# Performance work log

Hardware: AMD Instinct MI355X
Metric: run time of the kernel (lower is better)

Reference implementation:

```python
import jax, jax.numpy as jnp
import numpy as np

B, T, N = 32, 24, 512
DIM_IN, DIM_OUT, HID, EMB = 64, 2, 128, 16
NEG_SLOPE = 0.01  # nn.LeakyReLU default


def leaky_relu(x):
    return jnp.where(x >= 0, x, NEG_SLOPE * x)


def setup_inputs() -> dict:
    key = jax.random.key(0)
    ks = jax.random.split(key, 11)
    return {
        "eb": jax.random.normal(ks[0], (B, T, N, DIM_IN), jnp.float32),
        "time_eb": jax.random.normal(ks[1], (B, T, EMB), jnp.float32),
        "node_eb": jax.random.normal(ks[2], (N, EMB), jnp.float32),
        # ln1: Linear(dim_in, hidden) stored as [dim_in, hidden] (x @ W + b)
        "W1": jax.random.normal(ks[3], (DIM_IN, HID), jnp.float32) / np.sqrt(DIM_IN),
        "b1": jax.random.normal(ks[4], (HID,), jnp.float32) * 0.01,
        # ln3: Linear(hidden, dim_out)
        "W3": jax.random.normal(ks[5], (HID, DIM_OUT), jnp.float32) / np.sqrt(HID),
        "b3": jax.random.normal(ks[6], (DIM_OUT,), jnp.float32) * 0.01,
        "weights_pool_spa": jax.random.normal(ks[7], (EMB, HID, HID), jnp.float32),
        "bias_pool_spa": jax.random.normal(ks[8], (EMB, HID), jnp.float32),
        "weights_pool_tem": jax.random.normal(ks[9], (EMB, HID, HID), jnp.float32),
        "bias_pool_tem": jax.random.normal(ks[10], (EMB, HID), jnp.float32),
    }


def reference(eb, time_eb, node_eb, W1, b1, W3, b3,
              weights_pool_spa, bias_pool_spa,
              weights_pool_tem, bias_pool_tem):
    # eb: [b,t,n,dim_in] -> [b,t,n,hidden]
    eb_out = eb @ W1 + b1
    # spatial hypernetwork: per-node weight [n,hid,hid] and bias [n,hid]
    weights_spa = jnp.einsum('nd,dio->nio', node_eb, weights_pool_spa)
    bias_spa = node_eb @ bias_pool_spa  # [n,hid]
    out_spa = leaky_relu(jnp.einsum('btni,nio->btno', eb_out, weights_spa) + bias_spa)
    # temporal hypernetwork: per-(b,t) weight [b,t,hid,hid] and bias [b,t,1,hid]
    weights_tem = jnp.einsum('btd,dio->btio', time_eb, weights_pool_tem)
    bias_tem = (time_eb @ bias_pool_tem)[:, :, None, :]
    out_tem = leaky_relu(jnp.einsum('btni,btio->btno', out_spa, weights_tem) + bias_tem)
    logits = out_tem @ W3 + b3  # [b,t,n,dim_out]
    return logits
```

## Files before the change

### kernel.cpp

```cpp
#include <hip/hip_runtime.h>
#include <hip/hip_bf16.h>
#include <stdint.h>

#define BT   768
#define NN   512
#define DIN  64
#define HID  128
#define EMB  16
#define SLOPE 0.01f

typedef __attribute__((ext_vector_type(8))) short bf16x8;
typedef __attribute__((ext_vector_type(4))) float f32x4;
typedef __attribute__((ext_vector_type(4))) short short4v;

__device__ __forceinline__ short f2bf(float f) {
    uint32_t u = __float_as_uint(f);
    u += 0x7fff + ((u >> 16) & 1);
    return (short)(u >> 16);
}
__device__ __forceinline__ float bf2f(short s) {
    return __uint_as_float(((uint32_t)(unsigned short)s) << 16);
}

static const size_t OFF_PTT  = 0;
static const size_t OFF_PTS2 = 524288;
static const size_t OFF_QB   = 786432;
static const size_t OFF_H2   = 1048576;

__global__ __launch_bounds__(256)
void k_prep(const float* __restrict__ pool_spa, const float* __restrict__ pool_tem,
            const float* __restrict__ W1, const float* __restrict__ b1,
            const float* __restrict__ bp_spa,
            short* __restrict__ ptt, short* __restrict__ pts2,
            float* __restrict__ qb)
{
    const int b = blockIdx.x, t = threadIdx.x;
    __shared__ short smem[26112];

    if (b < 64) {
        const int d = b >> 2, o0 = (b & 3) * 32;
        short* s = smem;
        #pragma unroll
        for (int c = 0; c < 16; ++c) {
            int e = c * 256 + t;
            int i = e >> 5, oo = e & 31;
            s[oo * 136 + i] = f2bf(pool_tem[(d * HID + i) * HID + o0 + oo]);
        }
        __syncthreads();
        #pragma unroll
        for (int c = 0; c < 8; ++c) {
            int e = c * 256 + t;
            int oo = e >> 6, ii = (e & 63) * 2;
            uint32_t lo = (unsigned short)s[oo * 136 + ii];
            uint32_t hi = (unsigned short)s[oo * 136 + ii + 1];
            ((uint32_t*)ptt)[((d * HID + o0 + oo) * HID + ii) >> 1] = lo | (hi << 16);
        }
        return;
    }
    if (b < 66) {
        const int dbase = (b - 64) * 8;
        if (t < 128) {
            float a[8];
            #pragma unroll
            for (int dd = 0; dd < 8; ++dd) a[dd] = bp_spa[(dbase + dd) * HID + t];
            for (int i = 0; i < HID; ++i) {
                float bv = b1[i];
                #pragma unroll
                for (int dd = 0; dd < 8; ++dd)
                    a[dd] += bv * pool_spa[((dbase + dd) * HID + i) * HID + t];
            }
            #pragma unroll
            for (int dd = 0; dd < 8; ++dd) qb[(dbase + dd) * HID + t] = a[dd];
        }
        return;
    }
    {
        const int d = b - 66;
        const int wave = t >> 6, lane = t & 63, quad = lane >> 4, l15 = lane & 15;
        const int m0 = wave * 32;
        short* sPT  = smem;
        short* sW1b = smem + 128 * 136;
        #pragma unroll
        for (int c = 0; c < 64; ++c) {
            int idx = c * 256 + t;
            int i = idx >> 7, o = idx & 127;
            sPT[o * 136 + i] = f2bf(pool_spa[(d * HID + i) * HID + o]);
        }
        #pragma unroll
        for (int c = 0; c < 32; ++c) {
            int idx = c * 256 + t;
            sW1b[(idx >> 7) * 136 + (idx & 127)] = f2bf(W1[idx]);
        }
        __syncthreads();
        f32x4 acc[2][4] = {};
        #pragma unroll
        for (int kc = 0; kc < 4; ++kc) {
            bf16x8 a0 = *(const bf16x8*)(sPT + (m0 + l15) * 136 + kc * 32 + quad * 8);
            bf16x8 a1 = *(const bf16x8*)(sPT + (m0 + 16 + l15) * 136 + kc * 32 + quad * 8);
            #pragma unroll
            for (int tc = 0; tc < 4; ++tc) {
                bf16x8 bb = *(const bf16x8*)(sW1b + (tc * 16 + l15) * 136 + kc * 32 + quad * 8);
                acc[0][tc] = __builtin_amdgcn_mfma_f32_16x16x32_bf16(a0, bb, acc[0][tc], 0, 0, 0);
                acc[1][tc] = __builtin_amdgcn_mfma_f32_16x16x32_bf16(a1, bb, acc[1][tc], 0, 0, 0);
            }
        }
        __syncthreads();
        short* sO = smem;
        #pragma unroll
        for (int tr = 0; tr < 2; ++tr)
            #pragma unroll
            for (int tc = 0; tc < 4; ++tc)
                #pragma unroll
                for (int r = 0; r < 4; ++r)
                    sO[(m0 + tr * 16 + quad * 4 + r) * 72 + tc * 16 + l15] = f2bf(acc[tr][tc][r]);
        __syncthreads();
        #pragma unroll
        for (int c = 0; c < 4; ++c) {
            int idx = c * 256 + t;
            int row = idx >> 3, ko = (idx & 7) * 8;
            *(bf16x8*)(pts2 + (size_t)d * 8192 + row * 64 + ko) =
                *(const bf16x8*)(sO + row * 72 + ko);
        }
    }
}

__global__ __launch_bounds__(256)
void k_spatial(const float* __restrict__ eb, const short* __restrict__ pts2,
               const float* __restrict__ qb, const float* __restrict__ node_eb,
               short* __restrict__ h2)
{
    const int n = blockIdx.x;
    const int t = threadIdx.x;
    const int wave = t >> 6, lane = t & 63, quad = lane >> 4, l15 = lane & 15;
    const int m0 = (wave >> 1) * 32, n0 = (wave & 1) * 64;

    __shared__ short sW[128 * 72];
    __shared__ short sEb[2][64 * 72];
    __shared__ short sOut[2][64 * 136];

    const float* ebn = eb + (size_t)n * DIN;
    short* h2n = h2 + (size_t)n * (BT * HID);

    float4 ev[4];
    #pragma unroll
    for (int c = 0; c < 4; ++c) {
        int idx = c * 256 + t;
        int r = idx >> 4, kq = (idx & 15) * 4;
        ev[c] = *(const float4*)(ebn + (size_t)r * (NN * DIN) + kq);
    }
    float ne[EMB];
    #pragma unroll
    for (int d = 0; d < EMB; ++d) ne[d] = node_eb[n * EMB + d];
    float bsr[4];
    #pragma unroll
    for (int tc = 0; tc < 4; ++tc) {
        int col = n0 + tc * 16 + l15;
        float a = 0.f;
        #pragma unroll
        for (int d = 0; d < EMB; ++d) a += ne[d] * qb[d * HID + col];
        bsr[tc] = a;
    }
    #pragma unroll
    for (int c = 0; c < 4; ++c) {
        int idx = c * 256 + t;
        int o = idx >> 3, k0 = (idx & 7) * 8;
        float a8[8] = {};
        #pragma unroll
        for (int d = 0; d < EMB; ++d) {
            bf16x8 pv = *(const bf16x8*)(pts2 + (size_t)d * 8192 + o * 64 + k0);
            #pragma unroll
            for (int e = 0; e < 8; ++e) a8[e] += ne[d] * bf2f(pv[e]);
        }
        bf16x8 w;
        #pragma unroll
        for (int e = 0; e < 8; ++e) w[e] = f2bf(a8[e]);
        *(bf16x8*)(sW + o * 72 + k0) = w;
    }
    #pragma unroll
    for (int c = 0; c < 4; ++c) {
        int idx = c * 256 + t;
        int r = idx >> 4, kq = (idx & 15) * 4;
        short4v s;
        s.x = f2bf(ev[c].x); s.y = f2bf(ev[c].y);
        s.z = f2bf(ev[c].z); s.w = f2bf(ev[c].w);
        *(short4v*)(sEb[0] + r * 72 + kq) = s;
    }
    __syncthreads();

    for (int ch = 0; ch < 12; ++ch) {
        const int cur = ch & 1, nxt = cur ^ 1;
        if (ch < 11) {
            #pragma unroll
            for (int c = 0; c < 4; ++c) {
                int idx = c * 256 + t;
                int r = (ch + 1) * 64 + (idx >> 4), kq = (idx & 15) * 4;
                ev[c] = *(const float4*)(ebn + (size_t)r * (NN * DIN) + kq);
            }
        }
        f32x4 acc[2][4] = {};
        #pragma unroll
        for (int kc = 0; kc < 2; ++kc) {
            bf16x8 a0 = *(const bf16x8*)(sEb[cur] + (m0 + l15) * 72 + kc * 32 + quad * 8);
            bf16x8 a1 = *(const bf16x8*)(sEb[cur] + (m0 + 16 + l15) * 72 + kc * 32 + quad * 8);
            #pragma unroll
            for (int tc = 0; tc < 4; ++tc) {
                bf16x8 bfr = *(const bf16x8*)(sW + (n0 + tc * 16 + l15) * 72 + kc * 32 + quad * 8);
                acc[0][tc] = __builtin_amdgcn_mfma_f32_16x16x32_bf16(a0, bfr, acc[0][tc], 0, 0, 0);
                acc[1][tc] = __builtin_amdgcn_mfma_f32_16x16x32_bf16(a1, bfr, acc[1][tc], 0, 0, 0);
            }
        }
        #pragma unroll
        for (int tr = 0; tr < 2; ++tr)
            #pragma unroll
            for (int tc = 0; tc < 4; ++tc) {
                int col = n0 + tc * 16 + l15;
                #pragma unroll
                for (int r = 0; r < 4; ++r) {
                    float v = acc[tr][tc][r] + bsr[tc];
                    v = (v >= 0.f) ? v : SLOPE * v;
                    sOut[cur][(m0 + tr * 16 + quad * 4 + r) * 136 + col] = f2bf(v);
                }
            }
        if (ch < 11) {
            #pragma unroll
            for (int c = 0; c < 4; ++c) {
                int idx = c * 256 + t;
                int r = idx >> 4, kq = (idx & 15) * 4;
                short4v s;
                s.x = f2bf(ev[c].x); s.y = f2bf(ev[c].y);
                s.z = f2bf(ev[c].z); s.w = f2bf(ev[c].w);
                *(short4v*)(sEb[nxt] + r * 72 + kq) = s;
            }
        }
        __syncthreads();
        #pragma unroll
        for (int c = 0; c < 4; ++c) {
            int idx = c * 256 + t;
            *(bf16x8*)(h2n + (size_t)ch * (64 * HID) + (size_t)idx * 8) =
                *(const bf16x8*)(sOut[cur] + (idx >> 4) * 136 + (idx & 15) * 8);
        }
    }
}

__global__ __launch_bounds__(256, 3)
void k_temporal(const short* __restrict__ h2, const short* __restrict__ ptt,
                const float* __restrict__ bp_tem, const float* __restrict__ time_eb,
                const float* __restrict__ W3, const float* __restrict__ b3,
                float* __restrict__ out)
{
    const int R = blockIdx.x;
    const int t = threadIdx.x;
    const int wave = t >> 6, lane = t & 63, quad = lane >> 4, l15 = lane & 15;
    const int m0 = wave * 16;

    __shared__ short sWt[128 * 136];
    __shared__ short sH2[64 * 136];

    const short* hb = h2 + (size_t)R * HID;

    bf16x8 hreg[4];
    #pragma unroll
    for (int c = 0; c < 4; ++c) {
        int idx = c * 256 + t;
        hreg[c] = *(const bf16x8*)(hb + (size_t)(idx >> 4) * (BT * HID) + (idx & 15) * 8);
    }
    float te[EMB];
    #pragma unroll
    for (int d = 0; d < EMB; ++d) te[d] = time_eb[R * EMB + d];
    #pragma unroll
    for (int c = 0; c < 8; ++c) {
        int idx = c * 256 + t;
        int o = idx >> 4, i0 = (idx & 15) * 8;
        float a8[8] = {};
        #pragma unroll
        for (int d = 0; d < EMB; ++d) {
            bf16x8 pv = *(const bf16x8*)(ptt + (size_t)d * 16384 + o * 128 + i0);
            #pragma unroll
            for (int e = 0; e < 8; ++e) a8[e] += te[d] * bf2f(pv[e]);
        }
        bf16x8 w;
        #pragma unroll
        for (int e = 0; e < 8; ++e) w[e] = f2bf(a8[e]);
        *(bf16x8*)(sWt + o * 136 + i0) = w;
    }
    float btr[8], w3r0[8], w3r1[8];
    #pragma unroll
    for (int tc = 0; tc < 8; ++tc) {
        int o = tc * 16 + l15;
        float a = 0.f;
        #pragma unroll
        for (int d = 0; d < EMB; ++d) a += te[d] * bp_tem[d * HID + o];
        btr[tc] = a;
        w3r0[tc] = W3[2 * o]; w3r1[tc] = W3[2 * o + 1];
    }
    const float b30 = b3[0], b31 = b3[1];

    #pragma unroll
    for (int c = 0; c < 4; ++c) {
        int idx = c * 256 + t;
        *(bf16x8*)(sH2 + (idx >> 4) * 136 + (idx & 15) * 8) = hreg[c];
    }
    __syncthreads();

    for (int nt = 0; nt < 8; ++nt) {
        if (nt < 7) {
            #pragma unroll
            for (int c = 0; c < 4; ++c) {
                int idx = c * 256 + t;
                hreg[c] = *(const bf16x8*)(hb + (size_t)((nt + 1) * 64 + (idx >> 4)) * (BT * HID) + (idx & 15) * 8);
            }
        }
        f32x4 acc[8] = {};
        #pragma unroll
        for (int kc = 0; kc < 4; ++kc) {
            bf16x8 a = *(const bf16x8*)(sH2 + (m0 + l15) * 136 + kc * 32 + quad * 8);
            #pragma unroll
            for (int tc = 0; tc < 8; ++tc) {
                bf16x8 b = *(const bf16x8*)(sWt + (tc * 16 + l15) * 136 + kc * 32 + quad * 8);
                acc[tc] = __builtin_amdgcn_mfma_f32_16x16x32_bf16(a, b, acc[tc], 0, 0, 0);
            }
        }
        float pl[4][2] = {};
        #pragma unroll
        for (int tc = 0; tc < 8; ++tc) {
            #pragma unroll
            for (int r = 0; r < 4; ++r) {
                float v = acc[tc][r] + btr[tc];
                v = (v >= 0.f) ? v : SLOPE * v;
                pl[r][0] += v * w3r0[tc];
                pl[r][1] += v * w3r1[tc];
            }
        }
        #pragma unroll
        for (int m = 1; m <= 8; m <<= 1)
            #pragma unroll
            for (int r = 0; r < 4; ++r) {
                pl[r][0] += __shfl_xor(pl[r][0], m);
                pl[r][1] += __shfl_xor(pl[r][1], m);
            }
        if (l15 == 0) {
            #pragma unroll
            for (int r = 0; r < 4; ++r) {
                int nrow = nt * 64 + m0 + quad * 4 + r;
                *(float2*)(out + ((size_t)R * NN + nrow) * 2) =
                    make_float2(pl[r][0] + b30, pl[r][1] + b31);
            }
        }
        __syncthreads();
        if (nt < 7) {
            #pragma unroll
            for (int c = 0; c < 4; ++c) {
                int idx = c * 256 + t;
                *(bf16x8*)(sH2 + (idx >> 4) * 136 + (idx & 15) * 8) = hreg[c];
            }
            __syncthreads();
        }
    }
}

extern "C" void kernel_launch(void* const* d_in, const int* in_sizes, int n_in,
                              void* d_out, int out_size, void* d_ws, size_t ws_size,
                              hipStream_t stream) {
    const float* eb        = (const float*)d_in[0];
    const float* time_eb   = (const float*)d_in[1];
    const float* node_eb   = (const float*)d_in[2];
    const float* W1        = (const float*)d_in[3];
    const float* b1        = (const float*)d_in[4];
    const float* W3        = (const float*)d_in[5];
    const float* b3        = (const float*)d_in[6];
    const float* pool_spa  = (const float*)d_in[7];
    const float* bpool_spa = (const float*)d_in[8];
    const float* pool_tem  = (const float*)d_in[9];
    const float* bpool_tem = (const float*)d_in[10];
    float* out = (float*)d_out;

    char* ws = (char*)d_ws;
    short* ptt  = (short*)(ws + OFF_PTT);
    short* pts2 = (short*)(ws + OFF_PTS2);
    float* qb   = (float*)(ws + OFF_QB);
    short* h2   = (short*)(ws + OFF_H2);

    k_prep<<<82, 256, 0, stream>>>(pool_spa, pool_tem, W1, b1, bpool_spa,
                                   ptt, pts2, qb);
    k_spatial<<<dim3(NN), 256, 0, stream>>>(eb, pts2, qb, node_eb, h2);
    k_temporal<<<dim3(BT), 256, 0, stream>>>(h2, ptt, bpool_tem, time_eb, W3, b3, out);
}
```

Baseline: 243.1 us.

## Process two nodes per spatial block and split BT rows across two blocks

Each spatial block now covers two adjacent nodes and half of the 768 BT rows, so every eb row load fetches 128 contiguous floats (two nodes) instead of 64. Each wave pair owns one node's generated weight matrix, and the grid becomes 256x2. The cost is that per-node weight generation is repeated in both row-halves, and a second barrier per chunk is added.

```diff
diff --git a/kernel.cpp b/kernel.cpp
--- a/kernel.cpp
+++ b/kernel.cpp
@@ -129,61 +129,65 @@
                const float* __restrict__ qb, const float* __restrict__ node_eb,
                short* __restrict__ h2)
 {
-    const int n = blockIdx.x;
+    const int n0 = blockIdx.x * 2;
+    const int Rbase = blockIdx.y * 384;
     const int t = threadIdx.x;
     const int wave = t >> 6, lane = t & 63, quad = lane >> 4, l15 = lane & 15;
-    const int m0 = (wave >> 1) * 32, n0 = (wave & 1) * 64;
-
-    __shared__ short sW[128 * 72];
-    __shared__ short sEb[2][64 * 72];
-    __shared__ short sOut[2][64 * 136];
-
-    const float* ebn = eb + (size_t)n * DIN;
-    short* h2n = h2 + (size_t)n * (BT * HID);
+    const int wn = wave >> 1;
+    const int mrow = (wave & 1) * 16;
+
+    __shared__ short sW[2][128 * 72];
+    __shared__ short sEb[2][2][32 * 72];
+    __shared__ short sOut[2][32 * 136];
+
+    const float* ebn = eb + (size_t)n0 * DIN;
 
     float4 ev[4];
     #pragma unroll
     for (int c = 0; c < 4; ++c) {
         int idx = c * 256 + t;
-        int r = idx >> 4, kq = (idx & 15) * 4;
-        ev[c] = *(const float4*)(ebn + (size_t)r * (NN * DIN) + kq);
+        int r = idx >> 5, f4 = idx & 31;
+        ev[c] = *(const float4*)(ebn + (size_t)(Rbase + r) * (NN * DIN) + f4 * 4);
     }
     float ne[EMB];
     #pragma unroll
-    for (int d = 0; d < EMB; ++d) ne[d] = node_eb[n * EMB + d];
-    float bsr[4];
-    #pragma unroll
-    for (int tc = 0; tc < 4; ++tc) {
-        int col = n0 + tc * 16 + l15;
+    for (int d = 0; d < EMB; ++d) ne[d] = node_eb[(n0 + wn) * EMB + d];
+    float bsr[8];
+    #pragma unroll
+    for (int tc = 0; tc < 8; ++tc) {
+        int col = tc * 16 + l15;
         float a = 0.f;
         #pragma unroll
         for (int d = 0; d < EMB; ++d) a += ne[d] * qb[d * HID + col];
         bsr[tc] = a;
     }
+    {
+        const int pt = t & 127;
+        #pragma unroll
+        for (int c = 0; c < 8; ++c) {
+            int cell = c * 128 + pt;
+            int o = cell >> 3, k0 = (cell & 7) * 8;
+            float a8[8] = {};
+            #pragma unroll
+            for (int d = 0; d < EMB; ++d) {
+                bf16x8 pv = *(const bf16x8*)(pts2 + (size_t)d * 8192 + o * 64 + k0);
+                #pragma unroll
+                for (int e = 0; e < 8; ++e) a8[e] += ne[d] * bf2f(pv[e]);
+            }
+            bf16x8 w;
+            #pragma unroll
+            for (int e = 0; e < 8; ++e) w[e] = f2bf(a8[e]);
+            *(bf16x8*)(&sW[wn][o * 72 + k0]) = w;
+        }
+    }
     #pragma unroll
     for (int c = 0; c < 4; ++c) {
         int idx = c * 256 + t;
-        int o = idx >> 3, k0 = (idx & 7) * 8;
-        float a8[8] = {};
-        #pragma unroll
-        for (int d = 0; d < EMB; ++d) {
-            bf16x8 pv = *(const bf16x8*)(pts2 + (size_t)d * 8192 + o * 64 + k0);
-            #pragma unroll
-            for (int e = 0; e < 8; ++e) a8[e] += ne[d] * bf2f(pv[e]);
-        }
-        bf16x8 w;
-        #pragma unroll
-        for (int e = 0; e < 8; ++e) w[e] = f2bf(a8[e]);
-        *(bf16x8*)(sW + o * 72 + k0) = w;
-    }
-    #pragma unroll
-    for (int c = 0; c < 4; ++c) {
-        int idx = c * 256 + t;
-        int r = idx >> 4, kq = (idx & 15) * 4;
+        int r = idx >> 5, nn = (idx & 31) >> 4, k4 = (idx & 15) * 4;
         short4v s;
         s.x = f2bf(ev[c].x); s.y = f2bf(ev[c].y);
         s.z = f2bf(ev[c].z); s.w = f2bf(ev[c].w);
-        *(short4v*)(sEb[0] + r * 72 + kq) = s;
+        *(short4v*)(&sEb[0][nn][r * 72 + k4]) = s;
     }
     __syncthreads();
 
@@ -193,52 +197,51 @@
             #pragma unroll
             for (int c = 0; c < 4; ++c) {
                 int idx = c * 256 + t;
-                int r = (ch + 1) * 64 + (idx >> 4), kq = (idx & 15) * 4;
-                ev[c] = *(const float4*)(ebn + (size_t)r * (NN * DIN) + kq);
-            }
-        }
-        f32x4 acc[2][4] = {};
+                int r = (ch + 1) * 32 + (idx >> 5), f4 = idx & 31;
+                ev[c] = *(const float4*)(ebn + (size_t)(Rbase + r) * (NN * DIN) + f4 * 4);
+            }
+        }
+        f32x4 acc[8] = {};
         #pragma unroll
         for (int kc = 0; kc < 2; ++kc) {
-            bf16x8 a0 = *(const bf16x8*)(sEb[cur] + (m0 + l15) * 72 + kc * 32 + quad * 8);
-            bf16x8 a1 = *(const bf16x8*)(sEb[cur] + (m0 + 16 + l15) * 72 + kc * 32 + quad * 8);
-            #pragma unroll
-            for (int tc = 0; tc < 4; ++tc) {
-                bf16x8 bfr = *(const bf16x8*)(sW + (n0 + tc * 16 + l15) * 72 + kc * 32 + quad * 8);
-                acc[0][tc] = __builtin_amdgcn_mfma_f32_16x16x32_bf16(a0, bfr, acc[0][tc], 0, 0, 0);
-                acc[1][tc] = __builtin_amdgcn_mfma_f32_16x16x32_bf16(a1, bfr, acc[1][tc], 0, 0, 0);
-            }
-        }
-        #pragma unroll
-        for (int tr = 0; tr < 2; ++tr)
-            #pragma unroll
-            for (int tc = 0; tc < 4; ++tc) {
-                int col = n0 + tc * 16 + l15;
-                #pragma unroll
-                for (int r = 0; r < 4; ++r) {
-                    float v = acc[tr][tc][r] + bsr[tc];
-                    v = (v >= 0.f) ? v : SLOPE * v;
-                    sOut[cur][(m0 + tr * 16 + quad * 4 + r) * 136 + col] = f2bf(v);
-                }
-            }
+            bf16x8 a = *(const bf16x8*)(&sEb[cur][wn][(mrow + l15) * 72 + kc * 32 + quad * 8]);
+            #pragma unroll
+            for (int tc = 0; tc < 8; ++tc) {
+                bf16x8 bfr = *(const bf16x8*)(&sW[wn][(tc * 16 + l15) * 72 + kc * 32 + quad * 8]);
+                acc[tc] = __builtin_amdgcn_mfma_f32_16x16x32_bf16(a, bfr, acc[tc], 0, 0, 0);
+            }
+        }
+        #pragma unroll
+        for (int tc = 0; tc < 8; ++tc) {
+            int col = tc * 16 + l15;
+            #pragma unroll
+            for (int r = 0; r < 4; ++r) {
+                float v = acc[tc][r] + bsr[tc];
+                v = (v >= 0.f) ? v : SLOPE * v;
+                sOut[wn][(mrow + quad * 4 + r) * 136 + col] = f2bf(v);
+            }
+        }
         if (ch < 11) {
             #pragma unroll
             for (int c = 0; c < 4; ++c) {
                 int idx = c * 256 + t;
-                int r = idx >> 4, kq = (idx & 15) * 4;
+                int r = idx >> 5, nn = (idx & 31) >> 4, k4 = (idx & 15) * 4;
                 short4v s;
                 s.x = f2bf(ev[c].x); s.y = f2bf(ev[c].y);
                 s.z = f2bf(ev[c].z); s.w = f2bf(ev[c].w);
-                *(short4v*)(sEb[nxt] + r * 72 + kq) = s;
+                *(short4v*)(&sEb[nxt][nn][r * 72 + k4]) = s;
             }
         }
         __syncthreads();
         #pragma unroll
         for (int c = 0; c < 4; ++c) {
             int idx = c * 256 + t;
-            *(bf16x8*)(h2n + (size_t)ch * (64 * HID) + (size_t)idx * 8) =
-                *(const bf16x8*)(sOut[cur] + (idx >> 4) * 136 + (idx & 15) * 8);
-        }
+            int ni = idx >> 9, row = (idx & 511) >> 4, col8 = (idx & 15) * 8;
+            *(bf16x8*)(h2 + (size_t)(n0 + ni) * (BT * HID)
+                          + (size_t)(Rbase + ch * 32 + row) * HID + col8) =
+                *(const bf16x8*)(&sOut[ni][row * 136 + col8]);
+        }
+        __syncthreads();
     }
 }
 
@@ -382,6 +385,6 @@
 
     k_prep<<<82, 256, 0, stream>>>(pool_spa, pool_tem, W1, b1, bpool_spa,
                                    ptt, pts2, qb);
-    k_spatial<<<dim3(NN), 256, 0, stream>>>(eb, pts2, qb, node_eb, h2);
+    k_spatial<<<dim3(256, 2), 256, 0, stream>>>(eb, pts2, qb, node_eb, h2);
     k_temporal<<<dim3(BT), 256, 0, stream>>>(h2, ptt, bpool_tem, time_eb, W3, b3, out);
 }
```

New measurement: 247.8 us. No clear change (+2.0%).

## Split spatial and temporal stages by node halves and co-schedule them in one mixed kernel

Applied to the files above, without the earlier changes.

The spatial stage is split so each block handles half of the 768 (b,t) rows for one node, and the temporal stage is split into two node halves. The first node half of the spatial work, plus the pool_tem transpose, runs first. A mixed kernel then interleaves the remaining spatial blocks with temporal blocks for the already finished node half, and a final kernel runs temporal work for the second half. The aim is to fill the GPU better and overlap the two stages, at the price of generating each per-node and per-(b,t) hypernetwork weight twice and using larger shared-memory blocks.

```diff
diff --git a/kernel.cpp b/kernel.cpp
--- a/kernel.cpp
+++ b/kernel.cpp
@@ -27,38 +27,275 @@
 static const size_t OFF_QB   = 786432;
 static const size_t OFF_H2   = 1048576;
 
+
+__device__ __forceinline__ void spatial_block(
+    const float* __restrict__ eb, const short* __restrict__ pts2,
+    const float* __restrict__ qb, const float* __restrict__ node_eb,
+    short* __restrict__ h2, short* smem, int n, int Rbase)
+{
+    const int t = threadIdx.x;
+    const int wave = t >> 6, lane = t & 63, quad = lane >> 4, l15 = lane & 15;
+    const int m0 = (wave >> 1) * 32, n0 = (wave & 1) * 64;
+
+    short* sW    = smem;
+    short* sEbB  = smem + 9216;
+    short* sOutB = smem + 18432;
+
+    const float* ebn = eb + (size_t)n * DIN;
+    short* h2n = h2 + (size_t)n * (BT * HID) + (size_t)Rbase * HID;
+
+    float4 ev[4];
+    #pragma unroll
+    for (int c = 0; c < 4; ++c) {
+        int idx = c * 256 + t;
+        int r = idx >> 4, kq = (idx & 15) * 4;
+        ev[c] = *(const float4*)(ebn + (size_t)(Rbase + r) * (NN * DIN) + kq);
+    }
+    float ne[EMB];
+    #pragma unroll
+    for (int d = 0; d < EMB; ++d) ne[d] = node_eb[n * EMB + d];
+    float bsr[4];
+    #pragma unroll
+    for (int tc = 0; tc < 4; ++tc) {
+        int col = n0 + tc * 16 + l15;
+        float a = 0.f;
+        #pragma unroll
+        for (int d = 0; d < EMB; ++d) a += ne[d] * qb[d * HID + col];
+        bsr[tc] = a;
+    }
+    #pragma unroll
+    for (int c = 0; c < 4; ++c) {
+        int idx = c * 256 + t;
+        int o = idx >> 3, k0 = (idx & 7) * 8;
+        float a8[8] = {};
+        #pragma unroll
+        for (int d = 0; d < EMB; ++d) {
+            bf16x8 pv = *(const bf16x8*)(pts2 + (size_t)d * 8192 + o * 64 + k0);
+            #pragma unroll
+            for (int e = 0; e < 8; ++e) a8[e] += ne[d] * bf2f(pv[e]);
+        }
+        bf16x8 w;
+        #pragma unroll
+        for (int e = 0; e < 8; ++e) w[e] = f2bf(a8[e]);
+        *(bf16x8*)(sW + o * 72 + k0) = w;
+    }
+    #pragma unroll
+    for (int c = 0; c < 4; ++c) {
+        int idx = c * 256 + t;
+        int r = idx >> 4, kq = (idx & 15) * 4;
+        short4v s;
+        s.x = f2bf(ev[c].x); s.y = f2bf(ev[c].y);
+        s.z = f2bf(ev[c].z); s.w = f2bf(ev[c].w);
+        *(short4v*)(sEbB + r * 72 + kq) = s;
+    }
+    __syncthreads();
+
+    for (int ch = 0; ch < 6; ++ch) {
+        const int cur = ch & 1;
+        short* se  = sEbB + cur * 4608;
+        short* snx = sEbB + (cur ^ 1) * 4608;
+        short* so  = sOutB + cur * 8704;
+        if (ch < 5) {
+            #pragma unroll
+            for (int c = 0; c < 4; ++c) {
+                int idx = c * 256 + t;
+                int r = (ch + 1) * 64 + (idx >> 4), kq = (idx & 15) * 4;
+                ev[c] = *(const float4*)(ebn + (size_t)(Rbase + r) * (NN * DIN) + kq);
+            }
+        }
+        f32x4 acc[2][4] = {};
+        #pragma unroll
+        for (int kc = 0; kc < 2; ++kc) {
+            bf16x8 a0 = *(const bf16x8*)(se + (m0 + l15) * 72 + kc * 32 + quad * 8);
+            bf16x8 a1 = *(const bf16x8*)(se + (m0 + 16 + l15) * 72 + kc * 32 + quad * 8);
+            #pragma unroll
+            for (int tc = 0; tc < 4; ++tc) {
+                bf16x8 bfr = *(const bf16x8*)(sW + (n0 + tc * 16 + l15) * 72 + kc * 32 + quad * 8);
+                acc[0][tc] = __builtin_amdgcn_mfma_f32_16x16x32_bf16(a0, bfr, acc[0][tc], 0, 0, 0);
+                acc[1][tc] = __builtin_amdgcn_mfma_f32_16x16x32_bf16(a1, bfr, acc[1][tc], 0, 0, 0);
+            }
+        }
+        #pragma unroll
+        for (int tr = 0; tr < 2; ++tr)
+            #pragma unroll
+            for (int tc = 0; tc < 4; ++tc) {
+                int col = n0 + tc * 16 + l15;
+                #pragma unroll
+                for (int r = 0; r < 4; ++r) {
+                    float v = acc[tr][tc][r] + bsr[tc];
+                    v = (v >= 0.f) ? v : SLOPE * v;
+                    so[(m0 + tr * 16 + quad * 4 + r) * 136 + col] = f2bf(v);
+                }
+            }
+        if (ch < 5) {
+            #pragma unroll
+            for (int c = 0; c < 4; ++c) {
+                int idx = c * 256 + t;
+                int r = idx >> 4, kq = (idx & 15) * 4;
+                short4v s;
+                s.x = f2bf(ev[c].x); s.y = f2bf(ev[c].y);
+                s.z = f2bf(ev[c].z); s.w = f2bf(ev[c].w);
+                *(short4v*)(snx + r * 72 + kq) = s;
+            }
+        }
+        __syncthreads();
+        #pragma unroll
+        for (int c = 0; c < 4; ++c) {
+            int idx = c * 256 + t;
+            *(bf16x8*)(h2n + (size_t)ch * (64 * HID) + (size_t)idx * 8) =
+                *(const bf16x8*)(so + (idx >> 4) * 136 + (idx & 15) * 8);
+        }
+    }
+}
+
+__device__ __forceinline__ void temporal_block(
+    const short* __restrict__ h2, const short* __restrict__ ptt,
+    const float* __restrict__ bp_tem, const float* __restrict__ time_eb,
+    const float* __restrict__ W3, const float* __restrict__ b3,
+    float* __restrict__ out, short* smem, int R, int ntBase)
+{
+    const int t = threadIdx.x;
+    const int wave = t >> 6, lane = t & 63, quad = lane >> 4, l15 = lane & 15;
+    const int m0 = wave * 16;
+    short* sWt = smem;
+    short* sH2 = smem + 17408;
+    const short* hb = h2 + (size_t)R * HID;
+
+    bf16x8 hreg[4];
+    #pragma unroll
+    for (int c = 0; c < 4; ++c) {
+        int idx = c * 256 + t;
+        hreg[c] = *(const bf16x8*)(hb + (size_t)(ntBase * 64 + (idx >> 4)) * (BT * HID) + (idx & 15) * 8);
+    }
+    float te[EMB];
+    #pragma unroll
+    for (int d = 0; d < EMB; ++d) te[d] = time_eb[R * EMB + d];
+    #pragma unroll
+    for (int c = 0; c < 8; ++c) {
+        int idx = c * 256 + t;
+        int o = idx >> 4, i0 = (idx & 15) * 8;
+        float a8[8] = {};
+        #pragma unroll
+        for (int d = 0; d < EMB; ++d) {
+            bf16x8 pv = *(const bf16x8*)(ptt + (size_t)d * 16384 + o * 128 + i0);
+            #pragma unroll
+            for (int e = 0; e < 8; ++e) a8[e] += te[d] * bf2f(pv[e]);
+        }
+        bf16x8 w;
+        #pragma unroll
+        for (int e = 0; e < 8; ++e) w[e] = f2bf(a8[e]);
+        *(bf16x8*)(sWt + o * 136 + i0) = w;
+    }
+    float btr[8], w3r0[8], w3r1[8];
+    #pragma unroll
+    for (int tc = 0; tc < 8; ++tc) {
+        int o = tc * 16 + l15;
+        float a = 0.f;
+        #pragma unroll
+        for (int d = 0; d < EMB; ++d) a += te[d] * bp_tem[d * HID + o];
+        btr[tc] = a;
+        w3r0[tc] = W3[2 * o]; w3r1[tc] = W3[2 * o + 1];
+    }
+    const float b30 = b3[0], b31 = b3[1];
+
+    #pragma unroll
+    for (int c = 0; c < 4; ++c) {
+        int idx = c * 256 + t;
+        *(bf16x8*)(sH2 + (idx >> 4) * 136 + (idx & 15) * 8) = hreg[c];
+    }
+    __syncthreads();
+
+    for (int j = 0; j < 4; ++j) {
+        const int nt = ntBase + j;
+        if (j < 3) {
+            #pragma unroll
+            for (int c = 0; c < 4; ++c) {
+                int idx = c * 256 + t;
+                hreg[c] = *(const bf16x8*)(hb + (size_t)((nt + 1) * 64 + (idx >> 4)) * (BT * HID) + (idx & 15) * 8);
+            }
+        }
+        f32x4 acc[8] = {};
+        #pragma unroll
+        for (int kc = 0; kc < 4; ++kc) {
+            bf16x8 a = *(const bf16x8*)(sH2 + (m0 + l15) * 136 + kc * 32 + quad * 8);
+            #pragma unroll
+            for (int tc = 0; tc < 8; ++tc) {
+                bf16x8 b = *(const bf16x8*)(sWt + (tc * 16 + l15) * 136 + kc * 32 + quad * 8);
+                acc[tc] = __builtin_amdgcn_mfma_f32_16x16x32_bf16(a, b, acc[tc], 0, 0, 0);
+            }
+        }
+        float pl[4][2] = {};
+        #pragma unroll
+        for (int tc = 0; tc < 8; ++tc) {
+            #pragma unroll
+            for (int r = 0; r < 4; ++r) {
+                float v = acc[tc][r] + btr[tc];
+                v = (v >= 0.f) ? v : SLOPE * v;
+                pl[r][0] += v * w3r0[tc];
+                pl[r][1] += v * w3r1[tc];
+            }
+        }
+        #pragma unroll
+        for (int m = 1; m <= 8; m <<= 1)
+            #pragma unroll
+            for (int r = 0; r < 4; ++r) {
+                pl[r][0] += __shfl_xor(pl[r][0], m);
+                pl[r][1] += __shfl_xor(pl[r][1], m);
+            }
+        if (l15 == 0) {
+            #pragma unroll
+            for (int r = 0; r < 4; ++r) {
+                int nrow = nt * 64 + m0 + quad * 4 + r;
+                *(float2*)(out + ((size_t)R * NN + nrow) * 2) =
+                    make_float2(pl[r][0] + b30, pl[r][1] + b31);
+            }
+        }
+        __syncthreads();
+        if (j < 3) {
+            #pragma unroll
+            for (int c = 0; c < 4; ++c) {
+                int idx = c * 256 + t;
+                *(bf16x8*)(sH2 + (idx >> 4) * 136 + (idx & 15) * 8) = hreg[c];
+            }
+            __syncthreads();
+        }
+    }
+}
+
+__device__ __forceinline__ void ptt_block(const float* __restrict__ pool_tem,
+                                          short* __restrict__ ptt,
+                                          short* s, int bb)
+{
+    const int t = threadIdx.x;
+    const int d = bb >> 2, o0 = (bb & 3) * 32;
+    #pragma unroll
+    for (int c = 0; c < 16; ++c) {
+        int e = c * 256 + t;
+        int i = e >> 5, oo = e & 31;
+        s[oo * 136 + i] = f2bf(pool_tem[(d * HID + i) * HID + o0 + oo]);
+    }
+    __syncthreads();
+    #pragma unroll
+    for (int c = 0; c < 8; ++c) {
+        int e = c * 256 + t;
+        int oo = e >> 6, ii = (e & 63) * 2;
+        uint32_t lo = (unsigned short)s[oo * 136 + ii];
+        uint32_t hi = (unsigned short)s[oo * 136 + ii + 1];
+        ((uint32_t*)ptt)[((d * HID + o0 + oo) * HID + ii) >> 1] = lo | (hi << 16);
+    }
+}
+
+
 __global__ __launch_bounds__(256)
-void k_prep(const float* __restrict__ pool_spa, const float* __restrict__ pool_tem,
-            const float* __restrict__ W1, const float* __restrict__ b1,
-            const float* __restrict__ bp_spa,
-            short* __restrict__ ptt, short* __restrict__ pts2,
-            float* __restrict__ qb)
+void k_prep(const float* __restrict__ pool_spa, const float* __restrict__ W1,
+            const float* __restrict__ b1, const float* __restrict__ bp_spa,
+            short* __restrict__ pts2, float* __restrict__ qb)
 {
     const int b = blockIdx.x, t = threadIdx.x;
     __shared__ short smem[26112];
 
-    if (b < 64) {
-        const int d = b >> 2, o0 = (b & 3) * 32;
-        short* s = smem;
-        #pragma unroll
-        for (int c = 0; c < 16; ++c) {
-            int e = c * 256 + t;
-            int i = e >> 5, oo = e & 31;
-            s[oo * 136 + i] = f2bf(pool_tem[(d * HID + i) * HID + o0 + oo]);
-        }
-        __syncthreads();
-        #pragma unroll
-        for (int c = 0; c < 8; ++c) {
-            int e = c * 256 + t;
-            int oo = e >> 6, ii = (e & 63) * 2;
-            uint32_t lo = (unsigned short)s[oo * 136 + ii];
-            uint32_t hi = (unsigned short)s[oo * 136 + ii + 1];
-            ((uint32_t*)ptt)[((d * HID + o0 + oo) * HID + ii) >> 1] = lo | (hi << 16);
-        }
-        return;
-    }
-    if (b < 66) {
-        const int dbase = (b - 64) * 8;
+    if (b < 2) {
+        const int dbase = b * 8;
         if (t < 128) {
             float a[8];
             #pragma unroll
@@ -75,7 +312,7 @@
         return;
     }
     {
-        const int d = b - 66;
+        const int d = b - 2;
         const int wave = t >> 6, lane = t & 63, quad = lane >> 4, l15 = lane & 15;
         const int m0 = wave * 32;
         short* sPT  = smem;
@@ -125,237 +362,46 @@
 }
 
 __global__ __launch_bounds__(256)
-void k_spatial(const float* __restrict__ eb, const short* __restrict__ pts2,
-               const float* __restrict__ qb, const float* __restrict__ node_eb,
-               short* __restrict__ h2)
-{
-    const int n = blockIdx.x;
-    const int t = threadIdx.x;
-    const int wave = t >> 6, lane = t & 63, quad = lane >> 4, l15 = lane & 15;
-    const int m0 = (wave >> 1) * 32, n0 = (wave & 1) * 64;
-
-    __shared__ short sW[128 * 72];
-    __shared__ short sEb[2][64 * 72];
-    __shared__ short sOut[2][64 * 136];
-
-    const float* ebn = eb + (size_t)n * DIN;
-    short* h2n = h2 + (size_t)n * (BT * HID);
-
-    float4 ev[4];
-    #pragma unroll
-    for (int c = 0; c < 4; ++c) {
-        int idx = c * 256 + t;
-        int r = idx >> 4, kq = (idx & 15) * 4;
-        ev[c] = *(const float4*)(ebn + (size_t)r * (NN * DIN) + kq);
-    }
-    float ne[EMB];
-    #pragma unroll
-    for (int d = 0; d < EMB; ++d) ne[d] = node_eb[n * EMB + d];
-    float bsr[4];
-    #pragma unroll
-    for (int tc = 0; tc < 4; ++tc) {
-        int col = n0 + tc * 16 + l15;
-        float a = 0.f;
-        #pragma unroll
-        for (int d = 0; d < EMB; ++d) a += ne[d] * qb[d * HID + col];
-        bsr[tc] = a;
-    }
-    #pragma unroll
-    for (int c = 0; c < 4; ++c) {
-        int idx = c * 256 + t;
-        int o = idx >> 3, k0 = (idx & 7) * 8;
-        float a8[8] = {};
-        #pragma unroll
-        for (int d = 0; d < EMB; ++d) {
-            bf16x8 pv = *(const bf16x8*)(pts2 + (size_t)d * 8192 + o * 64 + k0);
-            #pragma unroll
-            for (int e = 0; e < 8; ++e) a8[e] += ne[d] * bf2f(pv[e]);
-        }
-        bf16x8 w;
-        #pragma unroll
-        for (int e = 0; e < 8; ++e) w[e] = f2bf(a8[e]);
-        *(bf16x8*)(sW + o * 72 + k0) = w;
-    }
-    #pragma unroll
-    for (int c = 0; c < 4; ++c) {
-        int idx = c * 256 + t;
-        int r = idx >> 4, kq = (idx & 15) * 4;
-        short4v s;
-        s.x = f2bf(ev[c].x); s.y = f2bf(ev[c].y);
-        s.z = f2bf(ev[c].z); s.w = f2bf(ev[c].w);
-        *(short4v*)(sEb[0] + r * 72 + kq) = s;
-    }
-    __syncthreads();
-
-    for (int ch = 0; ch < 12; ++ch) {
-        const int cur = ch & 1, nxt = cur ^ 1;
-        if (ch < 11) {
-            #pragma unroll
-            for (int c = 0; c < 4; ++c) {
-                int idx = c * 256 + t;
-                int r = (ch + 1) * 64 + (idx >> 4), kq = (idx & 15) * 4;
-                ev[c] = *(const float4*)(ebn + (size_t)r * (NN * DIN) + kq);
-            }
-        }
-        f32x4 acc[2][4] = {};
-        #pragma unroll
-        for (int kc = 0; kc < 2; ++kc) {
-            bf16x8 a0 = *(const bf16x8*)(sEb[cur] + (m0 + l15) * 72 + kc * 32 + quad * 8);
-            bf16x8 a1 = *(const bf16x8*)(sEb[cur] + (m0 + 16 + l15) * 72 + kc * 32 + quad * 8);
-            #pragma unroll
-            for (int tc = 0; tc < 4; ++tc) {
-                bf16x8 bfr = *(const bf16x8*)(sW + (n0 + tc * 16 + l15) * 72 + kc * 32 + quad * 8);
-                acc[0][tc] = __builtin_amdgcn_mfma_f32_16x16x32_bf16(a0, bfr, acc[0][tc], 0, 0, 0);
-                acc[1][tc] = __builtin_amdgcn_mfma_f32_16x16x32_bf16(a1, bfr, acc[1][tc], 0, 0, 0);
-            }
-        }
-        #pragma unroll
-        for (int tr = 0; tr < 2; ++tr)
-            #pragma unroll
-            for (int tc = 0; tc < 4; ++tc) {
-                int col = n0 + tc * 16 + l15;
-                #pragma unroll
-                for (int r = 0; r < 4; ++r) {
-                    float v = acc[tr][tc][r] + bsr[tc];
-                    v = (v >= 0.f) ? v : SLOPE * v;
-                    sOut[cur][(m0 + tr * 16 + quad * 4 + r) * 136 + col] = f2bf(v);
-                }
-            }
-        if (ch < 11) {
-            #pragma unroll
-            for (int c = 0; c < 4; ++c) {
-                int idx = c * 256 + t;
-                int r = idx >> 4, kq = (idx & 15) * 4;
-                short4v s;
-                s.x = f2bf(ev[c].x); s.y = f2bf(ev[c].y);
-                s.z = f2bf(ev[c].z); s.w = f2bf(ev[c].w);
-                *(short4v*)(sEb[nxt] + r * 72 + kq) = s;
-            }
-        }
-        __syncthreads();
-        #pragma unroll
-        for (int c = 0; c < 4; ++c) {
-            int idx = c * 256 + t;
-            *(bf16x8*)(h2n + (size_t)ch * (64 * HID) + (size_t)idx * 8) =
-                *(const bf16x8*)(sOut[cur] + (idx >> 4) * 136 + (idx & 15) * 8);
-        }
+void k_sA(const float* __restrict__ eb, const short* __restrict__ pts2,
+          const float* __restrict__ qb, const float* __restrict__ node_eb,
+          const float* __restrict__ pool_tem, short* __restrict__ ptt,
+          short* __restrict__ h2)
+{
+    __shared__ short smem[35840];
+    const int b = blockIdx.x;
+    if (b < 64) { ptt_block(pool_tem, ptt, smem, b); return; }
+    const int sb = b - 64;
+    spatial_block(eb, pts2, qb, node_eb, h2, smem, sb >> 1, (sb & 1) * 384);
+}
+
+__global__ __launch_bounds__(256)
+void k_mix(const float* __restrict__ eb, const short* __restrict__ pts2,
+           const float* __restrict__ qb, const float* __restrict__ node_eb,
+           short* __restrict__ h2, const short* __restrict__ ptt,
+           const float* __restrict__ bp_tem, const float* __restrict__ time_eb,
+           const float* __restrict__ W3, const float* __restrict__ b3,
+           float* __restrict__ out)
+{
+    __shared__ short smem[35840];
+    const int b = blockIdx.x;
+    const int g = b / 5, r = b % 5;
+    if (r < 2) {
+        const int sb = g * 2 + r;
+        spatial_block(eb, pts2, qb, node_eb, h2, smem, 256 + (sb >> 1), (sb & 1) * 384);
+    } else {
+        const int R = g * 3 + (r - 2);
+        temporal_block(h2, ptt, bp_tem, time_eb, W3, b3, out, smem, R, 0);
     }
 }
 
 __global__ __launch_bounds__(256, 3)
-void k_temporal(const short* __restrict__ h2, const short* __restrict__ ptt,
-                const float* __restrict__ bp_tem, const float* __restrict__ time_eb,
-                const float* __restrict__ W3, const float* __restrict__ b3,
-                float* __restrict__ out)
-{
-    const int R = blockIdx.x;
-    const int t = threadIdx.x;
-    const int wave = t >> 6, lane = t & 63, quad = lane >> 4, l15 = lane & 15;
-    const int m0 = wave * 16;
-
-    __shared__ short sWt[128 * 136];
-    __shared__ short sH2[64 * 136];
-
-    const short* hb = h2 + (size_t)R * HID;
-
-    bf16x8 hreg[4];
-    #pragma unroll
-    for (int c = 0; c < 4; ++c) {
-        int idx = c * 256 + t;
-        hreg[c] = *(const bf16x8*)(hb + (size_t)(idx >> 4) * (BT * HID) + (idx & 15) * 8);
-    }
-    float te[EMB];
-    #pragma unroll
-    for (int d = 0; d < EMB; ++d) te[d] = time_eb[R * EMB + d];
-    #pragma unroll
-    for (int c = 0; c < 8; ++c) {
-        int idx = c * 256 + t;
-        int o = idx >> 4, i0 = (idx & 15) * 8;
-        float a8[8] = {};
-        #pragma unroll
-        for (int d = 0; d < EMB; ++d) {
-            bf16x8 pv = *(const bf16x8*)(ptt + (size_t)d * 16384 + o * 128 + i0);
-            #pragma unroll
-            for (int e = 0; e < 8; ++e) a8[e] += te[d] * bf2f(pv[e]);
-        }
-        bf16x8 w;
-        #pragma unroll
-        for (int e = 0; e < 8; ++e) w[e] = f2bf(a8[e]);
-        *(bf16x8*)(sWt + o * 136 + i0) = w;
-    }
-    float btr[8], w3r0[8], w3r1[8];
-    #pragma unroll
-    for (int tc = 0; tc < 8; ++tc) {
-        int o = tc * 16 + l15;
-        float a = 0.f;
-        #pragma unroll
-        for (int d = 0; d < EMB; ++d) a += te[d] * bp_tem[d * HID + o];
-        btr[tc] = a;
-        w3r0[tc] = W3[2 * o]; w3r1[tc] = W3[2 * o + 1];
-    }
-    const float b30 = b3[0], b31 = b3[1];
-
-    #pragma unroll
-    for (int c = 0; c < 4; ++c) {
-        int idx = c * 256 + t;
-        *(bf16x8*)(sH2 + (idx >> 4) * 136 + (idx & 15) * 8) = hreg[c];
-    }
-    __syncthreads();
-
-    for (int nt = 0; nt < 8; ++nt) {
-        if (nt < 7) {
-            #pragma unroll
-            for (int c = 0; c < 4; ++c) {
-                int idx = c * 256 + t;
-                hreg[c] = *(const bf16x8*)(hb + (size_t)((nt + 1) * 64 + (idx >> 4)) * (BT * HID) + (idx & 15) * 8);
-            }
-        }
-        f32x4 acc[8] = {};
-        #pragma unroll
-        for (int kc = 0; kc < 4; ++kc) {
-            bf16x8 a = *(const bf16x8*)(sH2 + (m0 + l15) * 136 + kc * 32 + quad * 8);
-            #pragma unroll
-            for (int tc = 0; tc < 8; ++tc) {
-                bf16x8 b = *(const bf16x8*)(sWt + (tc * 16 + l15) * 136 + kc * 32 + quad * 8);
-                acc[tc] = __builtin_amdgcn_mfma_f32_16x16x32_bf16(a, b, acc[tc], 0, 0, 0);
-            }
-        }
-        float pl[4][2] = {};
-        #pragma unroll
-        for (int tc = 0; tc < 8; ++tc) {
-            #pragma unroll
-            for (int r = 0; r < 4; ++r) {
-                float v = acc[tc][r] + btr[tc];
-                v = (v >= 0.f) ? v : SLOPE * v;
-                pl[r][0] += v * w3r0[tc];
-                pl[r][1] += v * w3r1[tc];
-            }
-        }
-        #pragma unroll
-        for (int m = 1; m <= 8; m <<= 1)
-            #pragma unroll
-            for (int r = 0; r < 4; ++r) {
-                pl[r][0] += __shfl_xor(pl[r][0], m);
-                pl[r][1] += __shfl_xor(pl[r][1], m);
-            }
-        if (l15 == 0) {
-            #pragma unroll
-            for (int r = 0; r < 4; ++r) {
-                int nrow = nt * 64 + m0 + quad * 4 + r;
-                *(float2*)(out + ((size_t)R * NN + nrow) * 2) =
-                    make_float2(pl[r][0] + b30, pl[r][1] + b31);
-            }
-        }
-        __syncthreads();
-        if (nt < 7) {
-            #pragma unroll
-            for (int c = 0; c < 4; ++c) {
-                int idx = c * 256 + t;
-                *(bf16x8*)(sH2 + (idx >> 4) * 136 + (idx & 15) * 8) = hreg[c];
-            }
-            __syncthreads();
-        }
-    }
+void k_tB(const short* __restrict__ h2, const short* __restrict__ ptt,
+          const float* __restrict__ bp_tem, const float* __restrict__ time_eb,
+          const float* __restrict__ W3, const float* __restrict__ b3,
+          float* __restrict__ out)
+{
+    __shared__ short smem[26112];
+    temporal_block(h2, ptt, bp_tem, time_eb, W3, b3, out, smem, blockIdx.x, 4);
 }
 
 extern "C" void kernel_launch(void* const* d_in, const int* in_sizes, int n_in,
@@ -380,8 +426,9 @@
     float* qb   = (float*)(ws + OFF_QB);
     short* h2   = (short*)(ws + OFF_H2);
 
-    k_prep<<<82, 256, 0, stream>>>(pool_spa, pool_tem, W1, b1, bpool_spa,
-                                   ptt, pts2, qb);
-    k_spatial<<<dim3(NN), 256, 0, stream>>>(eb, pts2, qb, node_eb, h2);
-    k_temporal<<<dim3(BT), 256, 0, stream>>>(h2, ptt, bpool_tem, time_eb, W3, b3, out);
-}
+    k_prep<<<18, 256, 0, stream>>>(pool_spa, W1, b1, bpool_spa, pts2, qb);
+    k_sA<<<576, 256, 0, stream>>>(eb, pts2, qb, node_eb, pool_tem, ptt, h2);
+    k_mix<<<1280, 256, 0, stream>>>(eb, pts2, qb, node_eb, h2, ptt, bpool_tem,
+                                    time_eb, W3, b3, out);
+    k_tB<<<768, 256, 0, stream>>>(h2, ptt, bpool_tem, time_eb, W3, b3, out);
+}
```

Result: slower. 272.2 us (+12.0%).
